# Optimization experiments

Hardware: AMD Instinct MI355X
Metric: run time of the kernel (lower is better)

The kernel has to match this reference:

```python
import jax, jax.numpy as jnp
import numpy as np

B, T, I = 256, 512, 64
INTER, CMD, MOTOR = 306, 204, 2  # AutoNCP(512, 2) layer sizes
UNITS = INTER + CMD + MOTOR


def _cell(xin, h, w1, b1, w2, b2, taw, tab, tbw, tbb, mask):
    # ncps CfCCell, mode='default', no backbone, ts=1.0
    x = jnp.concatenate([xin, h], axis=1)          # (B, in+n)
    m = mask.astype(x.dtype)                        # sparsity applied to ff weights
    ff1 = jnp.tanh(x @ (w1 * m).T + b1)
    ff2 = jnp.tanh(x @ (w2 * m).T + b2)
    t = jax.nn.sigmoid(-(x @ taw.T + tab) + (x @ tbw.T + tbb))
    return ff1 * (1.0 - t) + t * ff2


def setup_inputs() -> dict:
    key = jax.random.key(0)
    ks = jax.random.split(key, 32)
    layer_in = [I, INTER, CMD]
    layer_n = [INTER, CMD, MOTOR]
    inp = {}
    inp["x"] = jax.random.normal(ks[0], (B, T, I), dtype=jnp.float32)
    inp["h0"] = jnp.zeros((B, UNITS), dtype=jnp.float32)
    k = 1
    for l in range(3):
        fin, n = layer_in[l], layer_n[l]
        d = fin + n
        for name in ("ff1", "ff2", "ta", "tb"):
            inp[f"{name}_w{l}"] = jax.random.normal(ks[k], (n, d), dtype=jnp.float32) / np.float32(np.sqrt(d)); k += 1
            inp[f"{name}_b{l}"] = jnp.zeros((n,), dtype=jnp.float32)
        # NCP wiring: sparse input block (~0.5 density), dense (all-ones) recurrent block
        sparse = (jax.random.uniform(ks[k], (n, fin)) < 0.5).astype(jnp.int32); k += 1
        inp[f"mask{l}"] = jnp.concatenate([sparse, jnp.ones((n, n), jnp.int32)], axis=1)
    inp["fc_w"] = jax.random.normal(ks[k], (MOTOR, MOTOR), dtype=jnp.float32) / np.float32(np.sqrt(MOTOR))
    inp["fc_b"] = jnp.zeros((MOTOR,), dtype=jnp.float32)
    return inp


def reference(x, h0,
              ff1_w0, ff1_b0, ff2_w0, ff2_b0, ta_w0, ta_b0, tb_w0, tb_b0, mask0,
              ff1_w1, ff1_b1, ff2_w1, ff2_b1, ta_w1, ta_b1, tb_w1, tb_b1, mask1,
              ff1_w2, ff1_b2, ff2_w2, ff2_b2, ta_w2, ta_b2, tb_w2, tb_b2, mask2,
              fc_w, fc_b):
    p0 = (ff1_w0, ff1_b0, ff2_w0, ff2_b0, ta_w0, ta_b0, tb_w0, tb_b0, mask0)
    p1 = (ff1_w1, ff1_b1, ff2_w1, ff2_b1, ta_w1, ta_b1, tb_w1, tb_b1, mask1)
    p2 = (ff1_w2, ff1_b2, ff2_w2, ff2_b2, ta_w2, ta_b2, tb_w2, tb_b2, mask2)
    # hidden ordered [inter, command, motor] as in WiredCfCCell
    carry0 = (h0[:, :INTER], h0[:, INTER:INTER + CMD], h0[:, INTER + CMD:])

    def step(carry, xt):
        hi, hc, hm = carry
        hi = _cell(xt, hi, *p0)   # sensory -> inter
        hc = _cell(hi, hc, *p1)   # inter   -> command
        hm = _cell(hc, hm, *p2)   # command -> motor
        return (hi, hc, hm), None

    (hi, hc, hm), _ = jax.lax.scan(step, carry0, jnp.swapaxes(x, 0, 1))
    predictions = hm @ fc_w.T + fc_b   # fc_out on last-step motor output
    h = jnp.concatenate([hi, hc, hm], axis=1)
    return predictions, h
```

## Files before the change

### kernel.cpp

```cpp
#include <hip/hip_runtime.h>
#include <hip/hip_fp16.h>

typedef unsigned int u32;
typedef _Float16 h2v __attribute__((ext_vector_type(2)));

#define TSLEN 512
#define N0 306
#define N1 204
#define D0 370
#define D1 510
#define D2 206

#define OFF_WA  0
#define OFF_WB  176256
#define OFF_WC1 332928
#define OFF_WC2 333344
#define OFF_WCT 333760
#define OFF_BA  334176
#define OFF_BB  335400
#define OFF_B2  336216

__device__ __forceinline__ u32 packh2(float a, float b) {
  __half2 h = __floats2half2_rn(a, b);
  return __builtin_bit_cast(u32, h);
}

__device__ __forceinline__ float dot2(u32 w, u32 xx, float acc) {
  return __builtin_amdgcn_fdot2(__builtin_bit_cast(h2v, w), __builtin_bit_cast(h2v, xx), acc, false);
}

__device__ __forceinline__ float cellact3(float a1, float a2, float at, float4 b) {
  float t1 = tanhf(a1 + b.x);
  float t2 = tanhf(a2 + b.y);
  float tv = 1.f / (1.f + __expf(-(at + b.z)));
  return t1 * (1.f - tv) + tv * t2;
}

template<int STR>
__device__ __forceinline__ float dot8(const uint4* __restrict__ wp, const uint4 (&xv)[8], float a) {
  uint4 wv[8];
  #pragma unroll
  for (int j = 0; j < 8; ++j) wv[j] = wp[j * STR];
  #pragma unroll
  for (int j = 0; j < 8; ++j) {
    a = dot2(wv[j].x, xv[j].x, a);
    a = dot2(wv[j].y, xv[j].y, a);
    a = dot2(wv[j].z, xv[j].z, a);
    a = dot2(wv[j].w, xv[j].w, a);
  }
  return a;
}

__global__ __launch_bounds__(256) void prep_kernel(
    const float* __restrict__ f1w0, const float* __restrict__ f2w0,
    const float* __restrict__ taw0, const float* __restrict__ tbw0, const int* __restrict__ m0,
    const float* __restrict__ f1b0, const float* __restrict__ f2b0,
    const float* __restrict__ tab0, const float* __restrict__ tbb0,
    const float* __restrict__ f1w1, const float* __restrict__ f2w1,
    const float* __restrict__ taw1, const float* __restrict__ tbw1, const int* __restrict__ m1,
    const float* __restrict__ f1b1, const float* __restrict__ f2b1,
    const float* __restrict__ tab1, const float* __restrict__ tbb1,
    const float* __restrict__ f1w2, const float* __restrict__ f2w2,
    const float* __restrict__ taw2, const float* __restrict__ tbw2, const int* __restrict__ m2,
    const float* __restrict__ f1b2, const float* __restrict__ f2b2,
    const float* __restrict__ tab2, const float* __restrict__ tbb2,
    float* __restrict__ ws)
{
  int j = blockIdx.x * 256 + threadIdx.x;
  u32* W = (u32*)ws;
  if (j < 176256) {
    int q4 = j >> 2, c = j & 3;
    int jq = q4 / 918, us = q4 - jq * 918;
    int u = us / 3, s = us - u * 3;
    int plane = jq >> 4, jj = jq & 15;
    int p = s * 64 + jj * 4 + c;
    int k0 = 2 * p, k1 = 2 * p + 1;
    float v0 = 0.f, v1 = 0.f;
    if (k0 < D0) {
      int i = u * D0 + k0;
      v0 = (plane == 0) ? f1w0[i] * (float)m0[i]
         : (plane == 1) ? f2w0[i] * (float)m0[i]
                        : tbw0[i] - taw0[i];
    }
    if (k1 < D0) {
      int i = u * D0 + k1;
      v1 = (plane == 0) ? f1w0[i] * (float)m0[i]
         : (plane == 1) ? f2w0[i] * (float)m0[i]
                        : tbw0[i] - taw0[i];
    }
    W[OFF_WA + j] = packh2(v0, v1);
    return;
  }
  j -= 176256;
  if (j < 156672) {
    int q4 = j >> 2, c = j & 3;
    int jq = q4 / 816, us = q4 - jq * 816;
    int u = us >> 2, s = us & 3;
    int plane = jq >> 4, jj = jq & 15;
    int p = s * 64 + jj * 4 + c;
    int k0 = 2 * p, k1 = 2 * p + 1;
    float v0 = 0.f, v1 = 0.f;
    if (k0 < D1) {
      int i = u * D1 + k0;
      v0 = (plane == 0) ? f1w1[i] * (float)m1[i]
         : (plane == 1) ? f2w1[i] * (float)m1[i]
                        : tbw1[i] - taw1[i];
    }
    if (k1 < D1) {
      int i = u * D1 + k1;
      v1 = (plane == 0) ? f1w1[i] * (float)m1[i]
         : (plane == 1) ? f2w1[i] * (float)m1[i]
                        : tbw1[i] - taw1[i];
    }
    W[OFF_WB + j] = packh2(v0, v1);
    return;
  }
  j -= 156672;
  if (j < 416) {
    int u = j / 208, d = j - u * 208;
    float f1 = 0.f, f2 = 0.f, td = 0.f;
    if (d < D2) { int i = u * D2 + d; float m = (float)m2[i]; f1 = f1w2[i]*m; f2 = f2w2[i]*m; td = tbw2[i]-taw2[i]; }
    ws[OFF_WC1 + j] = f1; ws[OFF_WC2 + j] = f2; ws[OFF_WCT + j] = td;
    return;
  }
  j -= 416;
  if (j < 306) { ((float4*)(ws + OFF_BA))[j] = make_float4(f1b0[j], f2b0[j], tbb0[j] - tab0[j], 0.f); return; }
  j -= 306;
  if (j < 204) { ((float4*)(ws + OFF_BB))[j] = make_float4(f1b1[j], f2b1[j], tbb1[j] - tab1[j], 0.f); return; }
  j -= 204;
  if (j < 2)   { ((float4*)(ws + OFF_B2))[j] = make_float4(f1b2[j], f2b2[j], tbb2[j] - tab2[j], 0.f); return; }
}

__global__ __launch_bounds__(1024, 1) void lnn_main(
    const float* __restrict__ x, const float* __restrict__ h0,
    const float* __restrict__ fcw, const float* __restrict__ fcb,
    const float* __restrict__ ws, float* __restrict__ out)
{
  __shared__ uint4 XA4[48];
  __shared__ uint4 XB4[64];
  __shared__ float XB32[512];
  __shared__ float pA[918 * 3];
  __shared__ float pB[204 * 13];
  __shared__ float shm2[2];

  const int tid = threadIdx.x;
  const int row = blockIdx.x;

  const int sA_ = tid % 3;
  const int uB = tid >> 2, sB_ = tid & 3;
  const int l15 = tid - 960, u2 = l15 & 1, ch = l15 >> 1;

  const uint4* __restrict__ WA4 = (const uint4*)((const u32*)ws + OFF_WA);
  const uint4* __restrict__ WB4 = (const uint4*)((const u32*)ws + OFF_WB);
  const float4* BA4 = (const float4*)(ws + OFF_BA);
  const float4* BB4 = (const float4*)(ws + OFF_BB);
  const float4* B24 = (const float4*)(ws + OFF_B2);

  __half* XAh = (__half*)XA4;
  __half* XBh = (__half*)XB4;

  float4 ba = make_float4(0.f,0.f,0.f,0.f), bb = make_float4(0.f,0.f,0.f,0.f), b2 = make_float4(0.f,0.f,0.f,0.f);
  float wc1[7], wc2[7], wct[7];
  float hm0 = 0.f, hm1 = 0.f;

  if (tid < 306) ba = BA4[tid];
  if (tid < 204) bb = BB4[tid];
  if (tid >= 960) {
    #pragma unroll
    for (int j = 0; j < 7; ++j) {
      int d = ch * 7 + j;
      bool ok = d < 208;
      wc1[j] = ok ? ws[OFF_WC1 + u2 * 208 + d] : 0.f;
      wc2[j] = ok ? ws[OFF_WC2 + u2 * 208 + d] : 0.f;
      wct[j] = ok ? ws[OFF_WCT + u2 * 208 + d] : 0.f;
    }
    b2 = B24[u2];
    hm0 = h0[(size_t)row * 512 + 510];
    hm1 = h0[(size_t)row * 512 + 511];
  }

  if (tid < 306) {
    float v = h0[(size_t)row * 512 + tid];
    XAh[64 + tid] = __float2half(v);
  }
  if (tid < 204) {
    float v = h0[(size_t)row * 512 + 306 + tid];
    XBh[306 + tid] = __float2half(v);
    XB32[306 + tid] = v;
  }
  if (tid < 14) XAh[370 + tid] = __float2half(0.f);
  if (tid >= 14 && tid < 16) XBh[510 + (tid - 14)] = __float2half(0.f);
  __syncthreads();

  for (int t = 0; t < TSLEN; ++t) {
    if (t > 0 && tid < 204) {
      int b = tid * 13;
      float a1 = pB[b+0] + pB[b+3] + pB[b+6] + pB[b+9];
      float a2 = pB[b+1] + pB[b+4] + pB[b+7] + pB[b+10];
      float at = pB[b+2] + pB[b+5] + pB[b+8] + pB[b+11];
      float hc = cellact3(a1, a2, at, bb);
      XB32[306 + tid] = hc;
      XBh[306 + tid] = __float2half(hc);
    } else if (tid >= 204 && tid < 236) {
      int i = tid - 204;
      float2 xv = *(const float2*)(x + ((size_t)row * TSLEN + t) * 64 + 2 * i);
      ((u32*)XA4)[i] = packh2(xv.x, xv.y);
    }
    __syncthreads();

    if (tid < 918) {
      const uint4* wp = WA4 + tid;
      const uint4* xs = XA4 + sA_ * 16;
      float a1 = 0.f, a2 = 0.f, at = 0.f;
      #pragma unroll
      for (int h = 0; h < 2; ++h) {
        uint4 xv[8];
        #pragma unroll
        for (int j = 0; j < 8; ++j) xv[j] = xs[h * 8 + j];
        a1 = dot8<918>(wp + (0 * 16 + h * 8) * 918, xv, a1);
        a2 = dot8<918>(wp + (1 * 16 + h * 8) * 918, xv, a2);
        at = dot8<918>(wp + (2 * 16 + h * 8) * 918, xv, at);
      }
      pA[tid * 3 + 0] = a1; pA[tid * 3 + 1] = a2; pA[tid * 3 + 2] = at;
    } else if (tid >= 960 && t > 0) {
      float a1 = 0.f, a2 = 0.f, at = 0.f;
      #pragma unroll
      for (int j = 0; j < 7; ++j) {
        int d = ch * 7 + j;
        float xv = (d < 204) ? XB32[306 + d] : (d == 204 ? hm0 : (d == 205 ? hm1 : 0.f));
        a1 = fmaf(wc1[j], xv, a1); a2 = fmaf(wc2[j], xv, a2); at = fmaf(wct[j], xv, at);
      }
      #pragma unroll
      for (int m = 2; m <= 32; m <<= 1) {
        a1 += __shfl_xor(a1, m); a2 += __shfl_xor(a2, m); at += __shfl_xor(at, m);
      }
      float hmn = cellact3(a1, a2, at, b2);
      float other = __shfl_xor(hmn, 1);
      hm0 = (u2 == 0) ? hmn : other;
      hm1 = (u2 == 0) ? other : hmn;
    }
    __syncthreads();

    if (tid < 306) {
      int b = tid * 9;
      float a1 = pA[b+0] + pA[b+3] + pA[b+6];
      float a2 = pA[b+1] + pA[b+4] + pA[b+7];
      float at = pA[b+2] + pA[b+5] + pA[b+8];
      float hi = cellact3(a1, a2, at, ba);
      XB32[tid] = hi;
      __half hh = __float2half(hi);
      XBh[tid] = hh;
      XAh[64 + tid] = hh;
    }
    __syncthreads();

    if (tid < 816) {
      const uint4* wp = WB4 + tid;
      const uint4* xs = XB4 + sB_ * 16;
      float a1 = 0.f, a2 = 0.f, at = 0.f;
      #pragma unroll
      for (int h = 0; h < 2; ++h) {
        uint4 xv[8];
        #pragma unroll
        for (int j = 0; j < 8; ++j) xv[j] = xs[h * 8 + j];
        a1 = dot8<816>(wp + (0 * 16 + h * 8) * 816, xv, a1);
        a2 = dot8<816>(wp + (1 * 16 + h * 8) * 816, xv, a2);
        at = dot8<816>(wp + (2 * 16 + h * 8) * 816, xv, at);
      }
      pB[uB * 13 + sB_ * 3 + 0] = a1;
      pB[uB * 13 + sB_ * 3 + 1] = a2;
      pB[uB * 13 + sB_ * 3 + 2] = at;
    }
    __syncthreads();
  }

  if (tid < 204) {
    int b = tid * 13;
    float a1 = pB[b+0] + pB[b+3] + pB[b+6] + pB[b+9];
    float a2 = pB[b+1] + pB[b+4] + pB[b+7] + pB[b+10];
    float at = pB[b+2] + pB[b+5] + pB[b+8] + pB[b+11];
    XB32[306 + tid] = cellact3(a1, a2, at, bb);
  }
  __syncthreads();
  if (tid >= 960) {
    float a1 = 0.f, a2 = 0.f, at = 0.f;
    #pragma unroll
    for (int j = 0; j < 7; ++j) {
      int d = ch * 7 + j;
      float xv = (d < 204) ? XB32[306 + d] : (d == 204 ? hm0 : (d == 205 ? hm1 : 0.f));
      a1 = fmaf(wc1[j], xv, a1); a2 = fmaf(wc2[j], xv, a2); at = fmaf(wct[j], xv, at);
    }
    #pragma unroll
    for (int m = 2; m <= 32; m <<= 1) {
      a1 += __shfl_xor(a1, m); a2 += __shfl_xor(a2, m); at += __shfl_xor(at, m);
    }
    float hmn = cellact3(a1, a2, at, b2);
    if (l15 < 2) shm2[u2] = hmn;
  }
  __syncthreads();

  if (tid < 2) {
    int o = tid;
    out[(size_t)row * 2 + o] = shm2[0] * fcw[o * 2 + 0] + shm2[1] * fcw[o * 2 + 1] + fcb[o];
  }
  if (tid < 512) {
    float v = (tid < 510) ? XB32[tid] : shm2[tid - 510];
    out[512 + (size_t)row * 512 + tid] = v;
  }
}

extern "C" void kernel_launch(void* const* d_in, const int* in_sizes, int n_in,
                              void* d_out, int out_size, void* d_ws, size_t ws_size,
                              hipStream_t stream) {
  const float* x    = (const float*)d_in[0];
  const float* h0   = (const float*)d_in[1];
  const float* f1w0 = (const float*)d_in[2];
  const float* f1b0 = (const float*)d_in[3];
  const float* f2w0 = (const float*)d_in[4];
  const float* f2b0 = (const float*)d_in[5];
  const float* taw0 = (const float*)d_in[6];
  const float* tab0 = (const float*)d_in[7];
  const float* tbw0 = (const float*)d_in[8];
  const float* tbb0 = (const float*)d_in[9];
  const int*   m0   = (const int*)d_in[10];
  const float* f1w1 = (const float*)d_in[11];
  const float* f1b1 = (const float*)d_in[12];
  const float* f2w1 = (const float*)d_in[13];
  const float* f2b1 = (const float*)d_in[14];
  const float* taw1 = (const float*)d_in[15];
  const float* tab1 = (const float*)d_in[16];
  const float* tbw1 = (const float*)d_in[17];
  const float* tbb1 = (const float*)d_in[18];
  const int*   m1   = (const int*)d_in[19];
  const float* f1w2 = (const float*)d_in[20];
  const float* f1b2 = (const float*)d_in[21];
  const float* f2w2 = (const float*)d_in[22];
  const float* f2b2 = (const float*)d_in[23];
  const float* taw2 = (const float*)d_in[24];
  const float* tab2 = (const float*)d_in[25];
  const float* tbw2 = (const float*)d_in[26];
  const float* tbb2 = (const float*)d_in[27];
  const int*   m2   = (const int*)d_in[28];
  const float* fcw  = (const float*)d_in[29];
  const float* fcb  = (const float*)d_in[30];

  float* ws  = (float*)d_ws;
  float* out = (float*)d_out;

  prep_kernel<<<1305, 256, 0, stream>>>(
      f1w0, f2w0, taw0, tbw0, m0, f1b0, f2b0, tab0, tbb0,
      f1w1, f2w1, taw1, tbw1, m1, f1b1, f2b1, tab1, tbb1,
      f1w2, f2w2, taw2, tbw2, m2, f1b2, f2b2, tab2, tbb2,
      ws);

  lnn_main<<<256, 1024, 0, stream>>>(x, h0, fcw, fcb, ws, out);
}
```

Before: 13.60 ms.

## Process four batch rows per block to reuse weight loads across rows

```diff
diff --git a/kernel.cpp b/kernel.cpp
--- a/kernel.cpp
+++ b/kernel.cpp
@@ -10,6 +10,7 @@
 #define D0 370
 #define D1 510
 #define D2 206
+#define RPB 4
 
 #define OFF_WA  0
 #define OFF_WB  176256
@@ -34,21 +35,6 @@
   float t2 = tanhf(a2 + b.y);
   float tv = 1.f / (1.f + __expf(-(at + b.z)));
   return t1 * (1.f - tv) + tv * t2;
-}
-
-template<int STR>
-__device__ __forceinline__ float dot8(const uint4* __restrict__ wp, const uint4 (&xv)[8], float a) {
-  uint4 wv[8];
-  #pragma unroll
-  for (int j = 0; j < 8; ++j) wv[j] = wp[j * STR];
-  #pragma unroll
-  for (int j = 0; j < 8; ++j) {
-    a = dot2(wv[j].x, xv[j].x, a);
-    a = dot2(wv[j].y, xv[j].y, a);
-    a = dot2(wv[j].z, xv[j].z, a);
-    a = dot2(wv[j].w, xv[j].w, a);
-  }
-  return a;
 }
 
 __global__ __launch_bounds__(256) void prep_kernel(
@@ -136,104 +122,125 @@
     const float* __restrict__ fcw, const float* __restrict__ fcb,
     const float* __restrict__ ws, float* __restrict__ out)
 {
-  __shared__ uint4 XA4[48];
-  __shared__ uint4 XB4[64];
-  __shared__ float XB32[512];
-  __shared__ float pA[918 * 3];
-  __shared__ float pB[204 * 13];
-  __shared__ float shm2[2];
+  __shared__ uint4 XA4[RPB][48];
+  __shared__ uint4 XB4[RPB][64];
+  __shared__ float XB32[RPB][512];
+  __shared__ float pA[RPB][2754];
+  __shared__ float pB[RPB][2652];
+  __shared__ float4 sBA[306];
+  __shared__ float4 sBB[204];
+  __shared__ float shm_hm[RPB][2];
 
   const int tid = threadIdx.x;
-  const int row = blockIdx.x;
-
-  const int sA_ = tid % 3;
-  const int uB = tid >> 2, sB_ = tid & 3;
-  const int l15 = tid - 960, u2 = l15 & 1, ch = l15 >> 1;
+  const int row0 = blockIdx.x * RPB;
+
+  const int sA3 = tid % 3;
+  const int sB4 = tid & 3;
 
   const uint4* __restrict__ WA4 = (const uint4*)((const u32*)ws + OFF_WA);
   const uint4* __restrict__ WB4 = (const uint4*)((const u32*)ws + OFF_WB);
-  const float4* BA4 = (const float4*)(ws + OFF_BA);
-  const float4* BB4 = (const float4*)(ws + OFF_BB);
-  const float4* B24 = (const float4*)(ws + OFF_B2);
-
-  __half* XAh = (__half*)XA4;
-  __half* XBh = (__half*)XB4;
-
-  float4 ba = make_float4(0.f,0.f,0.f,0.f), bb = make_float4(0.f,0.f,0.f,0.f), b2 = make_float4(0.f,0.f,0.f,0.f);
-  float wc1[7], wc2[7], wct[7];
+
+  __half* XAh = (__half*)&XA4[0][0];
+
+  const int l15 = tid - 960;
+  const int u2 = l15 & 1, r2c = (l15 >> 1) & 3, chc = l15 >> 3;
+  float4 b2 = make_float4(0.f, 0.f, 0.f, 0.f);
   float hm0 = 0.f, hm1 = 0.f;
-
-  if (tid < 306) ba = BA4[tid];
-  if (tid < 204) bb = BB4[tid];
   if (tid >= 960) {
-    #pragma unroll
-    for (int j = 0; j < 7; ++j) {
-      int d = ch * 7 + j;
-      bool ok = d < 208;
-      wc1[j] = ok ? ws[OFF_WC1 + u2 * 208 + d] : 0.f;
-      wc2[j] = ok ? ws[OFF_WC2 + u2 * 208 + d] : 0.f;
-      wct[j] = ok ? ws[OFF_WCT + u2 * 208 + d] : 0.f;
-    }
-    b2 = B24[u2];
-    hm0 = h0[(size_t)row * 512 + 510];
-    hm1 = h0[(size_t)row * 512 + 511];
-  }
-
-  if (tid < 306) {
-    float v = h0[(size_t)row * 512 + tid];
-    XAh[64 + tid] = __float2half(v);
-  }
-  if (tid < 204) {
-    float v = h0[(size_t)row * 512 + 306 + tid];
-    XBh[306 + tid] = __float2half(v);
-    XB32[306 + tid] = v;
-  }
-  if (tid < 14) XAh[370 + tid] = __float2half(0.f);
-  if (tid >= 14 && tid < 16) XBh[510 + (tid - 14)] = __float2half(0.f);
+    b2 = ((const float4*)(ws + OFF_B2))[u2];
+    hm0 = h0[(size_t)(row0 + r2c) * 512 + 510];
+    hm1 = h0[(size_t)(row0 + r2c) * 512 + 511];
+  }
+
+  if (tid < 306) sBA[tid] = ((const float4*)(ws + OFF_BA))[tid];
+  if (tid < 204) sBB[tid] = ((const float4*)(ws + OFF_BB))[tid];
+  for (int i = tid; i < RPB * N0; i += 1024) {
+    int u = i >> 2, r = i & 3;
+    ((__half*)XA4[r])[64 + u] = __float2half(h0[(size_t)(row0 + r) * 512 + u]);
+  }
+  for (int i = tid; i < RPB * N1; i += 1024) {
+    int u = i >> 2, r = i & 3;
+    ((__half*)XB4[r])[306 + u] = __float2half(h0[(size_t)(row0 + r) * 512 + 306 + u]);
+  }
+  if (tid < RPB * 14) {
+    int r = tid / 14, u = tid - r * 14;
+    ((__half*)XA4[r])[370 + u] = __float2half(0.f);
+  }
+  if (tid >= 64 && tid < 64 + RPB * 2) {
+    int i = tid - 64; int r = i >> 1;
+    ((__half*)XB4[r])[510 + (i & 1)] = __float2half(0.f);
+  }
   __syncthreads();
 
   for (int t = 0; t < TSLEN; ++t) {
-    if (t > 0 && tid < 204) {
-      int b = tid * 13;
-      float a1 = pB[b+0] + pB[b+3] + pB[b+6] + pB[b+9];
-      float a2 = pB[b+1] + pB[b+4] + pB[b+7] + pB[b+10];
-      float at = pB[b+2] + pB[b+5] + pB[b+8] + pB[b+11];
-      float hc = cellact3(a1, a2, at, bb);
-      XB32[306 + tid] = hc;
-      XBh[306 + tid] = __float2half(hc);
-    } else if (tid >= 204 && tid < 236) {
-      int i = tid - 204;
-      float2 xv = *(const float2*)(x + ((size_t)row * TSLEN + t) * 64 + 2 * i);
-      ((u32*)XA4)[i] = packh2(xv.x, xv.y);
+    if (tid < 816) {
+      if (t > 0) {
+        int u = tid >> 2, r = tid & 3;
+        const float* b = &pB[r][u * 13];
+        float a1 = b[0] + b[3] + b[6] + b[9];
+        float a2 = b[1] + b[4] + b[7] + b[10];
+        float at = b[2] + b[5] + b[8] + b[11];
+        float hc = cellact3(a1, a2, at, sBB[u]);
+        XB32[r][306 + u] = hc;
+        ((__half*)XB4[r])[306 + u] = __float2half(hc);
+      }
+    } else if (tid < 944) {
+      int i = tid - 816;
+      int r = i >> 5, jj = i & 31;
+      float2 xv = *(const float2*)(x + ((size_t)(row0 + r) * TSLEN + t) * 64 + 2 * jj);
+      ((u32*)XA4[r])[jj] = packh2(xv.x, xv.y);
     }
     __syncthreads();
 
     if (tid < 918) {
       const uint4* wp = WA4 + tid;
-      const uint4* xs = XA4 + sA_ * 16;
-      float a1 = 0.f, a2 = 0.f, at = 0.f;
+      float acc[3][RPB];
+      #pragma unroll
+      for (int p = 0; p < 3; ++p)
+        #pragma unroll
+        for (int r = 0; r < RPB; ++r) acc[p][r] = 0.f;
       #pragma unroll
       for (int h = 0; h < 2; ++h) {
-        uint4 xv[8];
         #pragma unroll
-        for (int j = 0; j < 8; ++j) xv[j] = xs[h * 8 + j];
-        a1 = dot8<918>(wp + (0 * 16 + h * 8) * 918, xv, a1);
-        a2 = dot8<918>(wp + (1 * 16 + h * 8) * 918, xv, a2);
-        at = dot8<918>(wp + (2 * 16 + h * 8) * 918, xv, at);
-      }
-      pA[tid * 3 + 0] = a1; pA[tid * 3 + 1] = a2; pA[tid * 3 + 2] = at;
+        for (int p = 0; p < 3; ++p) {
+          uint4 wv[8];
+          #pragma unroll
+          for (int j = 0; j < 8; ++j) wv[j] = wp[(p * 16 + h * 8 + j) * 918];
+          #pragma unroll
+          for (int r = 0; r < RPB; ++r) {
+            const uint4* xs = &XA4[r][sA3 * 16 + h * 8];
+            #pragma unroll
+            for (int j = 0; j < 8; ++j) {
+              uint4 xq = xs[j];
+              acc[p][r] = dot2(wv[j].x, xq.x, acc[p][r]);
+              acc[p][r] = dot2(wv[j].y, xq.y, acc[p][r]);
+              acc[p][r] = dot2(wv[j].z, xq.z, acc[p][r]);
+              acc[p][r] = dot2(wv[j].w, xq.w, acc[p][r]);
+            }
+          }
+        }
+      }
+      #pragma unroll
+      for (int r = 0; r < RPB; ++r) {
+        pA[r][tid * 3 + 0] = acc[0][r];
+        pA[r][tid * 3 + 1] = acc[1][r];
+        pA[r][tid * 3 + 2] = acc[2][r];
+      }
     } else if (tid >= 960 && t > 0) {
       float a1 = 0.f, a2 = 0.f, at = 0.f;
-      #pragma unroll
-      for (int j = 0; j < 7; ++j) {
-        int d = ch * 7 + j;
-        float xv = (d < 204) ? XB32[306 + d] : (d == 204 ? hm0 : (d == 205 ? hm1 : 0.f));
-        a1 = fmaf(wc1[j], xv, a1); a2 = fmaf(wc2[j], xv, a2); at = fmaf(wct[j], xv, at);
-      }
-      #pragma unroll
-      for (int m = 2; m <= 32; m <<= 1) {
-        a1 += __shfl_xor(a1, m); a2 += __shfl_xor(a2, m); at += __shfl_xor(at, m);
-      }
+      int dbase = chc * 26;
+      #pragma unroll
+      for (int j = 0; j < 26; ++j) {
+        int d = dbase + j;
+        float w1 = ws[OFF_WC1 + u2 * 208 + d];
+        float w2 = ws[OFF_WC2 + u2 * 208 + d];
+        float wt = ws[OFF_WCT + u2 * 208 + d];
+        float xv = (d < 204) ? XB32[r2c][306 + d] : (d == 204 ? hm0 : (d == 205 ? hm1 : 0.f));
+        a1 = fmaf(w1, xv, a1); a2 = fmaf(w2, xv, a2); at = fmaf(wt, xv, at);
+      }
+      a1 += __shfl_xor(a1, 8);  a2 += __shfl_xor(a2, 8);  at += __shfl_xor(at, 8);
+      a1 += __shfl_xor(a1, 16); a2 += __shfl_xor(a2, 16); at += __shfl_xor(at, 16);
+      a1 += __shfl_xor(a1, 32); a2 += __shfl_xor(a2, 32); at += __shfl_xor(at, 32);
       float hmn = cellact3(a1, a2, at, b2);
       float other = __shfl_xor(hmn, 1);
       hm0 = (u2 == 0) ? hmn : other;
@@ -241,71 +248,97 @@
     }
     __syncthreads();
 
-    if (tid < 306) {
-      int b = tid * 9;
-      float a1 = pA[b+0] + pA[b+3] + pA[b+6];
-      float a2 = pA[b+1] + pA[b+4] + pA[b+7];
-      float at = pA[b+2] + pA[b+5] + pA[b+8];
-      float hi = cellact3(a1, a2, at, ba);
-      XB32[tid] = hi;
+    for (int i = tid; i < RPB * N0; i += 1024) {
+      int u = i >> 2, r = i & 3;
+      const float* b = &pA[r][u * 9];
+      float a1 = b[0] + b[3] + b[6];
+      float a2 = b[1] + b[4] + b[7];
+      float at = b[2] + b[5] + b[8];
+      float hi = cellact3(a1, a2, at, sBA[u]);
+      XB32[r][u] = hi;
       __half hh = __float2half(hi);
-      XBh[tid] = hh;
-      XAh[64 + tid] = hh;
+      ((__half*)XB4[r])[u] = hh;
+      ((__half*)XA4[r])[64 + u] = hh;
     }
     __syncthreads();
 
     if (tid < 816) {
       const uint4* wp = WB4 + tid;
-      const uint4* xs = XB4 + sB_ * 16;
-      float a1 = 0.f, a2 = 0.f, at = 0.f;
+      int ub = tid >> 2;
+      float acc[3][RPB];
+      #pragma unroll
+      for (int p = 0; p < 3; ++p)
+        #pragma unroll
+        for (int r = 0; r < RPB; ++r) acc[p][r] = 0.f;
       #pragma unroll
       for (int h = 0; h < 2; ++h) {
-        uint4 xv[8];
         #pragma unroll
-        for (int j = 0; j < 8; ++j) xv[j] = xs[h * 8 + j];
-        a1 = dot8<816>(wp + (0 * 16 + h * 8) * 816, xv, a1);
-        a2 = dot8<816>(wp + (1 * 16 + h * 8) * 816, xv, a2);
-        at = dot8<816>(wp + (2 * 16 + h * 8) * 816, xv, at);
-      }
-      pB[uB * 13 + sB_ * 3 + 0] = a1;
-      pB[uB * 13 + sB_ * 3 + 1] = a2;
-      pB[uB * 13 + sB_ * 3 + 2] = at;
+        for (int p = 0; p < 3; ++p) {
+          uint4 wv[8];
+          #pragma unroll
+          for (int j = 0; j < 8; ++j) wv[j] = wp[(p * 16 + h * 8 + j) * 816];
+          #pragma unroll
+          for (int r = 0; r < RPB; ++r) {
+            const uint4* xs = &XB4[r][sB4 * 16 + h * 8];
+            #pragma unroll
+            for (int j = 0; j < 8; ++j) {
+              uint4 xq = xs[j];
+              acc[p][r] = dot2(wv[j].x, xq.x, acc[p][r]);
+              acc[p][r] = dot2(wv[j].y, xq.y, acc[p][r]);
+              acc[p][r] = dot2(wv[j].z, xq.z, acc[p][r]);
+              acc[p][r] = dot2(wv[j].w, xq.w, acc[p][r]);
+            }
+          }
+        }
+      }
+      #pragma unroll
+      for (int r = 0; r < RPB; ++r) {
+        pB[r][ub * 13 + sB4 * 3 + 0] = acc[0][r];
+        pB[r][ub * 13 + sB4 * 3 + 1] = acc[1][r];
+        pB[r][ub * 13 + sB4 * 3 + 2] = acc[2][r];
+      }
     }
     __syncthreads();
   }
 
-  if (tid < 204) {
-    int b = tid * 13;
-    float a1 = pB[b+0] + pB[b+3] + pB[b+6] + pB[b+9];
-    float a2 = pB[b+1] + pB[b+4] + pB[b+7] + pB[b+10];
-    float at = pB[b+2] + pB[b+5] + pB[b+8] + pB[b+11];
-    XB32[306 + tid] = cellact3(a1, a2, at, bb);
+  if (tid < 816) {
+    int u = tid >> 2, r = tid & 3;
+    const float* b = &pB[r][u * 13];
+    float a1 = b[0] + b[3] + b[6] + b[9];
+    float a2 = b[1] + b[4] + b[7] + b[10];
+    float at = b[2] + b[5] + b[8] + b[11];
+    XB32[r][306 + u] = cellact3(a1, a2, at, sBB[u]);
   }
   __syncthreads();
   if (tid >= 960) {
     float a1 = 0.f, a2 = 0.f, at = 0.f;
+    int dbase = chc * 26;
     #pragma unroll
-    for (int j = 0; j < 7; ++j) {
-      int d = ch * 7 + j;
-      float xv = (d < 204) ? XB32[306 + d] : (d == 204 ? hm0 : (d == 205 ? hm1 : 0.f));
-      a1 = fmaf(wc1[j], xv, a1); a2 = fmaf(wc2[j], xv, a2); at = fmaf(wct[j], xv, at);
-    }
-    #pragma unroll
-    for (int m = 2; m <= 32; m <<= 1) {
-      a1 += __shfl_xor(a1, m); a2 += __shfl_xor(a2, m); at += __shfl_xor(at, m);
-    }
+    for (int j = 0; j < 26; ++j) {
+      int d = dbase + j;
+      float w1 = ws[OFF_WC1 + u2 * 208 + d];
+      float w2 = ws[OFF_WC2 + u2 * 208 + d];
+      float wt = ws[OFF_WCT + u2 * 208 + d];
+      float xv = (d < 204) ? XB32[r2c][306 + d] : (d == 204 ? hm0 : (d == 205 ? hm1 : 0.f));
+      a1 = fmaf(w1, xv, a1); a2 = fmaf(w2, xv, a2); at = fmaf(wt, xv, at);
+    }
+    a1 += __shfl_xor(a1, 8);  a2 += __shfl_xor(a2, 8);  at += __shfl_xor(at, 8);
+    a1 += __shfl_xor(a1, 16); a2 += __shfl_xor(a2, 16); at += __shfl_xor(at, 16);
+    a1 += __shfl_xor(a1, 32); a2 += __shfl_xor(a2, 32); at += __shfl_xor(at, 32);
     float hmn = cellact3(a1, a2, at, b2);
-    if (l15 < 2) shm2[u2] = hmn;
+    if (chc == 0) shm_hm[r2c][u2] = hmn;
   }
   __syncthreads();
 
-  if (tid < 2) {
-    int o = tid;
-    out[(size_t)row * 2 + o] = shm2[0] * fcw[o * 2 + 0] + shm2[1] * fcw[o * 2 + 1] + fcb[o];
-  }
-  if (tid < 512) {
-    float v = (tid < 510) ? XB32[tid] : shm2[tid - 510];
-    out[512 + (size_t)row * 512 + tid] = v;
+  if (tid < 2 * RPB) {
+    int r = tid >> 1, o = tid & 1;
+    out[(size_t)(row0 + r) * 2 + o] =
+        shm_hm[r][0] * fcw[o * 2 + 0] + shm_hm[r][1] * fcw[o * 2 + 1] + fcb[o];
+  }
+  for (int i = tid; i < RPB * 512; i += 1024) {
+    int r = i >> 9, c = i & 511;
+    float v = (c < 510) ? XB32[r][c] : shm_hm[r][c - 510];
+    out[512 + (size_t)(row0 + r) * 512 + c] = v;
   }
 }
 
@@ -353,5 +386,5 @@
       f1w2, f2w2, taw2, tbw2, m2, f1b2, f2b2, tab2, tbb2,
       ws);
 
-  lnn_main<<<256, 1024, 0, stream>>>(x, h0, fcw, fcb, ws, out);
-}
+  lnn_main<<<64, 1024, 0, stream>>>(x, h0, fcw, fcb, ws, out);
+}
```

New measurement: 29.17 ms. +114.5%, slower.

## Double-buffer weight loads across phases and tighten register budget

Applied to the files above, without the earlier changes.

```diff
diff --git a/kernel.cpp b/kernel.cpp
--- a/kernel.cpp
+++ b/kernel.cpp
@@ -37,16 +37,17 @@
 }
 
 template<int STR>
-__device__ __forceinline__ float dot8(const uint4* __restrict__ wp, const uint4 (&xv)[8], float a) {
-  uint4 wv[8];
+__device__ __forceinline__ void load8(const uint4* __restrict__ p, uint4 (&w)[8]) {
   #pragma unroll
-  for (int j = 0; j < 8; ++j) wv[j] = wp[j * STR];
+  for (int j = 0; j < 8; ++j) w[j] = p[j * STR];
+}
+__device__ __forceinline__ float consume8(const uint4 (&w)[8], const uint4 (&xv)[8], float a) {
   #pragma unroll
   for (int j = 0; j < 8; ++j) {
-    a = dot2(wv[j].x, xv[j].x, a);
-    a = dot2(wv[j].y, xv[j].y, a);
-    a = dot2(wv[j].z, xv[j].z, a);
-    a = dot2(wv[j].w, xv[j].w, a);
+    a = dot2(w[j].x, xv[j].x, a);
+    a = dot2(w[j].y, xv[j].y, a);
+    a = dot2(w[j].z, xv[j].z, a);
+    a = dot2(w[j].w, xv[j].w, a);
   }
   return a;
 }
@@ -131,7 +132,7 @@
   if (j < 2)   { ((float4*)(ws + OFF_B2))[j] = make_float4(f1b2[j], f2b2[j], tbb2[j] - tab2[j], 0.f); return; }
 }
 
-__global__ __launch_bounds__(1024, 1) void lnn_main(
+__global__ __launch_bounds__(1024, 4) void lnn_main(
     const float* __restrict__ x, const float* __restrict__ h0,
     const float* __restrict__ fcw, const float* __restrict__ fcb,
     const float* __restrict__ ws, float* __restrict__ out)
@@ -159,22 +160,12 @@
   __half* XAh = (__half*)XA4;
   __half* XBh = (__half*)XB4;
 
-  float4 ba = make_float4(0.f,0.f,0.f,0.f), bb = make_float4(0.f,0.f,0.f,0.f), b2 = make_float4(0.f,0.f,0.f,0.f);
-  float wc1[7], wc2[7], wct[7];
+  float4 ba = make_float4(0.f,0.f,0.f,0.f), bb = make_float4(0.f,0.f,0.f,0.f);
   float hm0 = 0.f, hm1 = 0.f;
 
   if (tid < 306) ba = BA4[tid];
   if (tid < 204) bb = BB4[tid];
   if (tid >= 960) {
-    #pragma unroll
-    for (int j = 0; j < 7; ++j) {
-      int d = ch * 7 + j;
-      bool ok = d < 208;
-      wc1[j] = ok ? ws[OFF_WC1 + u2 * 208 + d] : 0.f;
-      wc2[j] = ok ? ws[OFF_WC2 + u2 * 208 + d] : 0.f;
-      wct[j] = ok ? ws[OFF_WCT + u2 * 208 + d] : 0.f;
-    }
-    b2 = B24[u2];
     hm0 = h0[(size_t)row * 512 + 510];
     hm1 = h0[(size_t)row * 512 + 511];
   }
@@ -191,6 +182,9 @@
   if (tid < 14) XAh[370 + tid] = __float2half(0.f);
   if (tid >= 14 && tid < 16) XBh[510 + (tid - 14)] = __float2half(0.f);
   __syncthreads();
+
+  uint4 wv0[8], wv1[8];
+  if (tid < 918) load8<918>(WA4 + tid, wv0);
 
   for (int t = 0; t < TSLEN; ++t) {
     if (t > 0 && tid < 204) {
@@ -203,37 +197,49 @@
       XBh[306 + tid] = __float2half(hc);
     } else if (tid >= 204 && tid < 236) {
       int i = tid - 204;
-      float2 xv = *(const float2*)(x + ((size_t)row * TSLEN + t) * 64 + 2 * i);
-      ((u32*)XA4)[i] = packh2(xv.x, xv.y);
+      float2 xv_ = *(const float2*)(x + ((size_t)row * TSLEN + t) * 64 + 2 * i);
+      ((u32*)XA4)[i] = packh2(xv_.x, xv_.y);
     }
     __syncthreads();
 
     if (tid < 918) {
       const uint4* wp = WA4 + tid;
       const uint4* xs = XA4 + sA_ * 16;
+      uint4 xv[8];
+      #pragma unroll
+      for (int j = 0; j < 8; ++j) xv[j] = xs[j];
+      load8<918>(wp + (1 * 16) * 918, wv1);
       float a1 = 0.f, a2 = 0.f, at = 0.f;
-      #pragma unroll
-      for (int h = 0; h < 2; ++h) {
-        uint4 xv[8];
-        #pragma unroll
-        for (int j = 0; j < 8; ++j) xv[j] = xs[h * 8 + j];
-        a1 = dot8<918>(wp + (0 * 16 + h * 8) * 918, xv, a1);
-        a2 = dot8<918>(wp + (1 * 16 + h * 8) * 918, xv, a2);
-        at = dot8<918>(wp + (2 * 16 + h * 8) * 918, xv, at);
-      }
+      a1 = consume8(wv0, xv, a1);
+      load8<918>(wp + (2 * 16) * 918, wv0);
+      a2 = consume8(wv1, xv, a2);
+      load8<918>(wp + (0 * 16 + 8) * 918, wv1);
+      at = consume8(wv0, xv, at);
+      load8<918>(wp + (1 * 16 + 8) * 918, wv0);
+      #pragma unroll
+      for (int j = 0; j < 8; ++j) xv[j] = xs[8 + j];
+      a1 = consume8(wv1, xv, a1);
+      load8<918>(wp + (2 * 16 + 8) * 918, wv1);
+      a2 = consume8(wv0, xv, a2);
+      at = consume8(wv1, xv, at);
       pA[tid * 3 + 0] = a1; pA[tid * 3 + 1] = a2; pA[tid * 3 + 2] = at;
     } else if (tid >= 960 && t > 0) {
       float a1 = 0.f, a2 = 0.f, at = 0.f;
       #pragma unroll
       for (int j = 0; j < 7; ++j) {
         int d = ch * 7 + j;
-        float xv = (d < 204) ? XB32[306 + d] : (d == 204 ? hm0 : (d == 205 ? hm1 : 0.f));
-        a1 = fmaf(wc1[j], xv, a1); a2 = fmaf(wc2[j], xv, a2); at = fmaf(wct[j], xv, at);
+        bool ok = d < 208;
+        float w1 = ok ? ws[OFF_WC1 + u2 * 208 + d] : 0.f;
+        float w2 = ok ? ws[OFF_WC2 + u2 * 208 + d] : 0.f;
+        float wt = ok ? ws[OFF_WCT + u2 * 208 + d] : 0.f;
+        float xv_ = (d < 204) ? XB32[306 + d] : (d == 204 ? hm0 : (d == 205 ? hm1 : 0.f));
+        a1 = fmaf(w1, xv_, a1); a2 = fmaf(w2, xv_, a2); at = fmaf(wt, xv_, at);
       }
       #pragma unroll
       for (int m = 2; m <= 32; m <<= 1) {
         a1 += __shfl_xor(a1, m); a2 += __shfl_xor(a2, m); at += __shfl_xor(at, m);
       }
+      float4 b2 = B24[u2];
       float hmn = cellact3(a1, a2, at, b2);
       float other = __shfl_xor(hmn, 1);
       hm0 = (u2 == 0) ? hmn : other;
@@ -241,6 +247,7 @@
     }
     __syncthreads();
 
+    if (tid < 816) load8<816>(WB4 + tid, wv0);
     if (tid < 306) {
       int b = tid * 9;
       float a1 = pA[b+0] + pA[b+3] + pA[b+6];
@@ -257,20 +264,28 @@
     if (tid < 816) {
       const uint4* wp = WB4 + tid;
       const uint4* xs = XB4 + sB_ * 16;
+      uint4 xv[8];
+      #pragma unroll
+      for (int j = 0; j < 8; ++j) xv[j] = xs[j];
+      load8<816>(wp + (1 * 16) * 816, wv1);
       float a1 = 0.f, a2 = 0.f, at = 0.f;
-      #pragma unroll
-      for (int h = 0; h < 2; ++h) {
-        uint4 xv[8];
-        #pragma unroll
-        for (int j = 0; j < 8; ++j) xv[j] = xs[h * 8 + j];
-        a1 = dot8<816>(wp + (0 * 16 + h * 8) * 816, xv, a1);
-        a2 = dot8<816>(wp + (1 * 16 + h * 8) * 816, xv, a2);
-        at = dot8<816>(wp + (2 * 16 + h * 8) * 816, xv, at);
-      }
+      a1 = consume8(wv0, xv, a1);
+      load8<816>(wp + (2 * 16) * 816, wv0);
+      a2 = consume8(wv1, xv, a2);
+      load8<816>(wp + (0 * 16 + 8) * 816, wv1);
+      at = consume8(wv0, xv, at);
+      load8<816>(wp + (1 * 16 + 8) * 816, wv0);
+      #pragma unroll
+      for (int j = 0; j < 8; ++j) xv[j] = xs[8 + j];
+      a1 = consume8(wv1, xv, a1);
+      load8<816>(wp + (2 * 16 + 8) * 816, wv1);
+      a2 = consume8(wv0, xv, a2);
+      at = consume8(wv1, xv, at);
       pB[uB * 13 + sB_ * 3 + 0] = a1;
       pB[uB * 13 + sB_ * 3 + 1] = a2;
       pB[uB * 13 + sB_ * 3 + 2] = at;
     }
+    if (tid < 918) load8<918>(WA4 + tid, wv0);
     __syncthreads();
   }
 
@@ -287,13 +302,18 @@
     #pragma unroll
     for (int j = 0; j < 7; ++j) {
       int d = ch * 7 + j;
-      float xv = (d < 204) ? XB32[306 + d] : (d == 204 ? hm0 : (d == 205 ? hm1 : 0.f));
-      a1 = fmaf(wc1[j], xv, a1); a2 = fmaf(wc2[j], xv, a2); at = fmaf(wct[j], xv, at);
+      bool ok = d < 208;
+      float w1 = ok ? ws[OFF_WC1 + u2 * 208 + d] : 0.f;
+      float w2 = ok ? ws[OFF_WC2 + u2 * 208 + d] : 0.f;
+      float wt = ok ? ws[OFF_WCT + u2 * 208 + d] : 0.f;
+      float xv_ = (d < 204) ? XB32[306 + d] : (d == 204 ? hm0 : (d == 205 ? hm1 : 0.f));
+      a1 = fmaf(w1, xv_, a1); a2 = fmaf(w2, xv_, a2); at = fmaf(wt, xv_, at);
     }
     #pragma unroll
     for (int m = 2; m <= 32; m <<= 1) {
       a1 += __shfl_xor(a1, m); a2 += __shfl_xor(a2, m); at += __shfl_xor(at, m);
     }
+    float4 b2 = B24[u2];
     float hmn = cellact3(a1, a2, at, b2);
     if (l15 < 2) shm2[u2] = hmn;
   }
```

Result: slower. 19.03 ms (+40.0%).
